# Performance work log

Measured on AMD Instinct MI355X. Metric: run time of the kernel, lower is better.

Reference implementation:

```python
import jax, jax.numpy as jnp
import numpy as np

N, D = 8192, 128

def setup_inputs() -> dict:
    key = jax.random.key(0)
    kq, kk, kv = jax.random.split(key, 3)
    query = jax.random.normal(kq, (N, D), dtype=jnp.float32)
    key_t = jax.random.normal(kk, (N, D), dtype=jnp.float32)
    value = jax.random.normal(kv, (N, D), dtype=jnp.float32)
    return {"query": query, "key": key_t, "value": value}

def reference(query, key, value):
    # FlashAttention-2 online softmax over blocks is mathematically exact
    # softmax attention: out = softmax(Q K^T / sqrt(d)) V, no mask.
    d = query.shape[-1]
    scale = 1.0 / jnp.sqrt(jnp.asarray(d, dtype=query.dtype))
    scores = jnp.einsum('qd,kd->qk', query, key) * scale  # [n, n]
    probs = jax.nn.softmax(scores, axis=-1)
    return jnp.einsum('qk,kd->qd', probs, value)  # [n, d]
```

## Files before the change

### kernel.cpp

```cpp
#include <hip/hip_runtime.h>
#include <hip/hip_bf16.h>

#define ATTN_N 8192
#define ATTN_D 128
#define TKEYS 128
#define NTILES (ATTN_N / TKEYS)
#define TILE_ELEMS (TKEYS * ATTN_D)
#define QROWS 64
#define KTPB 32

typedef __bf16 bf16_t;
typedef bf16_t bf16x2 __attribute__((ext_vector_type(2)));
typedef bf16_t bf16x8 __attribute__((ext_vector_type(8)));
typedef float f32x4 __attribute__((ext_vector_type(4)));

#if __has_builtin(__builtin_amdgcn_exp2f)
#define EXP2(x) __builtin_amdgcn_exp2f(x)
#else
#define EXP2(x) __expf((x) * 0.6931471805599453f)
#endif

__device__ __forceinline__ void dma16(const bf16_t* g, bf16_t* l) {
  __builtin_amdgcn_global_load_lds(
      (const __attribute__((address_space(1))) void*)g,
      (__attribute__((address_space(3))) void*)l, 16, 0, 0);
}

__global__ void prep_kernel(const float* __restrict__ q,
                            const float* __restrict__ k,
                            const float* __restrict__ v,
                            bf16_t* __restrict__ qb,
                            bf16_t* __restrict__ kswz,
                            bf16_t* __restrict__ vtswz) {
  __shared__ bf16_t tile[64][72];
  const int bk = blockIdx.x;
  const int bd = blockIdx.y;
  const int t = threadIdx.x;
  const float sc = 0.12751744f;

  const int row_l = t >> 2;
  const int key = bk * 64 + row_l;
  const int kt = key >> 7;
  const int r = key & 127;

#pragma unroll
  for (int u = 0; u < 2; ++u) {
    const int j = bd * 8 + (t & 3) * 2 + u;
    const float4* qs = (const float4*)(q + (size_t)key * ATTN_D + j * 8);
    const float4* ks = (const float4*)(k + (size_t)key * ATTN_D + j * 8);
    float4 a0 = qs[0], a1 = qs[1];
    float4 b0 = ks[0], b1 = ks[1];
    bf16x8 qo, ko;
    qo[0] = (bf16_t)(a0.x * sc); qo[1] = (bf16_t)(a0.y * sc);
    qo[2] = (bf16_t)(a0.z * sc); qo[3] = (bf16_t)(a0.w * sc);
    qo[4] = (bf16_t)(a1.x * sc); qo[5] = (bf16_t)(a1.y * sc);
    qo[6] = (bf16_t)(a1.z * sc); qo[7] = (bf16_t)(a1.w * sc);
    ko[0] = (bf16_t)b0.x; ko[1] = (bf16_t)b0.y;
    ko[2] = (bf16_t)b0.z; ko[3] = (bf16_t)b0.w;
    ko[4] = (bf16_t)b1.x; ko[5] = (bf16_t)b1.y;
    ko[6] = (bf16_t)b1.z; ko[7] = (bf16_t)b1.w;
    *(bf16x8*)(qb + (size_t)key * ATTN_D + j * 8) = qo;
    *(bf16x8*)(kswz + (size_t)kt * TILE_ELEMS + r * ATTN_D + (j ^ (r & 15)) * 8) = ko;
  }

  {
    const float* src = v + (size_t)key * ATTN_D + bd * 64 + (t & 3) * 16;
#pragma unroll
    for (int u = 0; u < 4; ++u) {
      float4 a = ((const float4*)src)[u];
      tile[row_l][(t & 3) * 16 + u * 4 + 0] = (bf16_t)a.x;
      tile[row_l][(t & 3) * 16 + u * 4 + 1] = (bf16_t)a.y;
      tile[row_l][(t & 3) * 16 + u * 4 + 2] = (bf16_t)a.z;
      tile[row_l][(t & 3) * 16 + u * 4 + 3] = (bf16_t)a.w;
    }
  }
  __syncthreads();
  {
    const int d_l = t >> 2;
    const int d = bd * 64 + d_l;
    const int h = bk & 1;
    const int ktv = bk >> 1;
#pragma unroll
    for (int u = 0; u < 2; ++u) {
      const int j = 8 * h + (t & 3) * 2 + u;
      bf16x8 o;
#pragma unroll
      for (int i = 0; i < 8; ++i) {
        const int key_tile = (j >> 2) * 32 + 4 * (j & 3) + (i >> 1) + 16 * (i & 1);
        o[i] = tile[key_tile - h * 64][d_l];
      }
      *(bf16x8*)(vtswz + (size_t)ktv * TILE_ELEMS + d * TKEYS + (j ^ (d & 15)) * 8) = o;
    }
  }
}

__global__ __launch_bounds__(512) void flash_attn_kernel(
    const bf16_t* __restrict__ qb, const bf16_t* __restrict__ kswz,
    const bf16_t* __restrict__ vtswz, float* __restrict__ partO,
    float* __restrict__ partL) {
  __shared__ __align__(16) bf16_t KV[2][2][TILE_ELEMS];
  __shared__ __align__(16) bf16_t Ps[8][32][40];
  __shared__ float cmb[8][32];
  float* Ob = (float*)&KV[0][0][0];

  const int t = threadIdx.x;
  const int w = t >> 6;
  const int lane = t & 63;
  const int quad = lane >> 4;
  const int col = lane & 15;
  const int rowHalf = w & 1;
  const int keyQ = w >> 1;
  const int blk = blockIdx.x;
  const int qg = blk >> 1;
  const int kh = blk & 1;
  const int q0 = qg * QROWS;
  const int ktbase = kh * KTPB;
  const int stg = ((blk >> 3) & 3) * 8;

  int offK[4][2], offV[8];
#pragma unroll
  for (int c = 0; c < 4; ++c)
#pragma unroll
    for (int cs = 0; cs < 2; ++cs)
      offK[c][cs] = (keyQ * 32 + cs * 16 + col) * ATTN_D +
                    (((c * 4 + quad) ^ col) * 8);
#pragma unroll
  for (int ds = 0; ds < 8; ++ds)
    offV[ds] = (ds * 16 + col) * TKEYS + (((keyQ * 4 + quad) ^ col) * 8);

  bf16x8 aq[2][4];
#pragma unroll
  for (int mi = 0; mi < 2; ++mi) {
    const int row = q0 + rowHalf * 32 + mi * 16 + col;
#pragma unroll
    for (int c = 0; c < 4; ++c)
      aq[mi][c] = *(const bf16x8*)(qb + (size_t)row * ATTN_D + c * 32 + quad * 8);
  }

  f32x4 oacc[2][8];
#pragma unroll
  for (int mi = 0; mi < 2; ++mi)
#pragma unroll
    for (int i = 0; i < 8; ++i) oacc[mi][i] = (f32x4){0.f, 0.f, 0.f, 0.f};
  float l_part[2][4] = {{0.f, 0.f, 0.f, 0.f}, {0.f, 0.f, 0.f, 0.f}};

  {
    const int kt = ktbase + (stg & (KTPB - 1));
    const bf16_t* kg = kswz + (size_t)kt * TILE_ELEMS + t * 8;
    const bf16_t* vg = vtswz + (size_t)kt * TILE_ELEMS + t * 8;
#pragma unroll
    for (int u = 0; u < 4; ++u) {
      dma16(kg + u * 4096, &KV[0][0][t * 8 + u * 4096]);
      dma16(vg + u * 4096, &KV[0][1][t * 8 + u * 4096]);
    }
  }
  __syncthreads();

  for (int it = 0; it < KTPB; ++it) {
    const int buf = it & 1;
    if (it + 1 < KTPB) {
      const int nt = ktbase + ((stg + it + 1) & (KTPB - 1));
      const bf16_t* kg = kswz + (size_t)nt * TILE_ELEMS + t * 8;
      const bf16_t* vg = vtswz + (size_t)nt * TILE_ELEMS + t * 8;
      bf16_t* kl = &KV[buf ^ 1][0][t * 8];
      bf16_t* vl = &KV[buf ^ 1][1][t * 8];
#pragma unroll
      for (int u = 0; u < 4; ++u) {
        dma16(kg + u * 4096, kl + u * 4096);
        dma16(vg + u * 4096, vl + u * 4096);
      }
    }
    const bf16_t* Kb = KV[buf][0];
    const bf16_t* Vb = KV[buf][1];

    f32x4 s[2][2];
#pragma unroll
    for (int mi = 0; mi < 2; ++mi)
#pragma unroll
      for (int ni = 0; ni < 2; ++ni) s[mi][ni] = (f32x4){0.f, 0.f, 0.f, 0.f};
#pragma unroll
    for (int c = 0; c < 4; ++c) {
      bf16x8 b0 = *(const bf16x8*)(Kb + offK[c][0]);
      bf16x8 b1 = *(const bf16x8*)(Kb + offK[c][1]);
      s[0][0] = __builtin_amdgcn_mfma_f32_16x16x32_bf16(aq[0][c], b0, s[0][0], 0, 0, 0);
      s[1][0] = __builtin_amdgcn_mfma_f32_16x16x32_bf16(aq[1][c], b0, s[1][0], 0, 0, 0);
      s[0][1] = __builtin_amdgcn_mfma_f32_16x16x32_bf16(aq[0][c], b1, s[0][1], 0, 0, 0);
      s[1][1] = __builtin_amdgcn_mfma_f32_16x16x32_bf16(aq[1][c], b1, s[1][1], 0, 0, 0);
    }

#pragma unroll
    for (int mi = 0; mi < 2; ++mi)
#pragma unroll
      for (int r = 0; r < 4; ++r) {
        float p0 = EXP2(s[mi][0][r]);
        float p1 = EXP2(s[mi][1][r]);
        l_part[mi][r] += p0 + p1;
        *(bf16x2*)&Ps[w][mi * 16 + quad * 4 + r][col * 2] =
            (bf16x2){(bf16_t)p0, (bf16_t)p1};
      }

    bf16x8 ap0 = *(const bf16x8*)&Ps[w][col][quad * 8];
    bf16x8 ap1 = *(const bf16x8*)&Ps[w][16 + col][quad * 8];
#pragma unroll
    for (int ds = 0; ds < 8; ++ds) {
      bf16x8 bv = *(const bf16x8*)(Vb + offV[ds]);
      oacc[0][ds] = __builtin_amdgcn_mfma_f32_16x16x32_bf16(ap0, bv, oacc[0][ds], 0, 0, 0);
      oacc[1][ds] = __builtin_amdgcn_mfma_f32_16x16x32_bf16(ap1, bv, oacc[1][ds], 0, 0, 0);
    }
    __syncthreads();
  }

#pragma unroll
  for (int mi = 0; mi < 2; ++mi)
#pragma unroll
    for (int r = 0; r < 4; ++r) {
      float v = l_part[mi][r];
#pragma unroll
      for (int off = 1; off < 16; off <<= 1)
        v += __shfl_xor(v, off, 64);
      if (col == 0) cmb[w][mi * 16 + quad * 4 + r] = v;
    }
  __syncthreads();
  if (t < QROWS) {
    const int rh = t >> 5, rl = t & 31;
    partL[(size_t)blk * QROWS + t] = cmb[rh][rl] + cmb[2 + rh][rl] +
                                     cmb[4 + rh][rl] + cmb[6 + rh][rl];
  }

#pragma unroll
  for (int p = 0; p < 4; ++p) {
    if (keyQ == p) {
#pragma unroll
      for (int mi = 0; mi < 2; ++mi)
#pragma unroll
        for (int ds = 0; ds < 8; ++ds)
#pragma unroll
          for (int r = 0; r < 4; ++r) {
            const int row = rowHalf * 32 + mi * 16 + quad * 4 + r;
            if (p == 0)
              Ob[row * 132 + ds * 16 + col] = oacc[mi][ds][r];
            else
              Ob[row * 132 + ds * 16 + col] += oacc[mi][ds][r];
          }
    }
    __syncthreads();
  }

  {
    float* dst = partO + (size_t)blk * (QROWS * ATTN_D);
    const int row = t >> 3;
    const int c0 = (t & 7) * 16;
#pragma unroll
    for (int u = 0; u < 4; ++u) {
      float4 vv = *(float4*)&Ob[row * 132 + c0 + u * 4];
      *(float4*)(dst + row * ATTN_D + c0 + u * 4) = vv;
    }
  }
}

__global__ void merge_kernel(const float* __restrict__ partO,
                             const float* __restrict__ partL,
                             float* __restrict__ out) {
  const int idx = blockIdx.x * blockDim.x + threadIdx.x;
  const int row = idx >> 5;
  const int gi = row >> 6;
  const int rl = row & 63;
  const int li = rl * 32 + (idx & 31);
  const float4* p0 = (const float4*)(partO + (size_t)(2 * gi) * (QROWS * ATTN_D));
  const float4* p1 = (const float4*)(partO + (size_t)(2 * gi + 1) * (QROWS * ATTN_D));
  const float invL = 1.0f / (partL[(size_t)(2 * gi) * QROWS + rl] +
                             partL[(size_t)(2 * gi + 1) * QROWS + rl]);
  float4 a = p0[li], b = p1[li], o;
  o.x = (a.x + b.x) * invL;
  o.y = (a.y + b.y) * invL;
  o.z = (a.z + b.z) * invL;
  o.w = (a.w + b.w) * invL;
  ((float4*)out)[idx] = o;
}

extern "C" void kernel_launch(void* const* d_in, const int* in_sizes, int n_in,
                              void* d_out, int out_size, void* d_ws, size_t ws_size,
                              hipStream_t stream) {
  const float* q = (const float*)d_in[0];
  const float* k = (const float*)d_in[1];
  const float* v = (const float*)d_in[2];
  float* out = (float*)d_out;

  bf16_t* qb = (bf16_t*)d_ws;
  bf16_t* kswz = qb + (size_t)ATTN_N * ATTN_D;
  bf16_t* vtswz = kswz + (size_t)ATTN_N * ATTN_D;
  float* partO = (float*)(vtswz + (size_t)ATTN_N * ATTN_D);
  float* partL = partO + (size_t)256 * QROWS * ATTN_D;

  prep_kernel<<<dim3(ATTN_N / 64, 2), 256, 0, stream>>>(q, k, v, qb, kswz, vtswz);
  flash_attn_kernel<<<256, 512, 0, stream>>>(qb, kswz, vtswz, partO, partL);
  merge_kernel<<<(ATTN_N * ATTN_D / 4) / 256, 256, 0, stream>>>(partO, partL, out);
}
```

Before: 123.9 us.

## Double query rows per block and split keys four ways

Each block now handles 128 query rows instead of 64, and the key range is split into 4 chunks instead of 2. This keeps the block count the same while each K/V tile in LDS is reused across twice as many query rows, which roughly halves K/V traffic per unit of work. The merge kernel now sums four partials. In exchange, per-thread accumulator registers double, which may reduce occupancy or cause spills, and the partial-output buffer and merge traffic grow.

```diff
diff --git a/kernel.cpp b/kernel.cpp
--- a/kernel.cpp
+++ b/kernel.cpp
@@ -6,8 +6,9 @@
 #define TKEYS 128
 #define NTILES (ATTN_N / TKEYS)
 #define TILE_ELEMS (TKEYS * ATTN_D)
-#define QROWS 64
-#define KTPB 32
+#define QROWS 128
+#define NSPLIT 4
+#define KTPB (NTILES / NSPLIT)
 
 typedef __bf16 bf16_t;
 typedef bf16_t bf16x2 __attribute__((ext_vector_type(2)));
@@ -100,7 +101,7 @@
     float* __restrict__ partL) {
   __shared__ __align__(16) bf16_t KV[2][2][TILE_ELEMS];
   __shared__ __align__(16) bf16_t Ps[8][32][40];
-  __shared__ float cmb[8][32];
+  __shared__ float cmb[8][64];
   float* Ob = (float*)&KV[0][0][0];
 
   const int t = threadIdx.x;
@@ -108,14 +109,14 @@
   const int lane = t & 63;
   const int quad = lane >> 4;
   const int col = lane & 15;
-  const int rowHalf = w & 1;
+  const int rowG = w & 1;
   const int keyQ = w >> 1;
   const int blk = blockIdx.x;
-  const int qg = blk >> 1;
-  const int kh = blk & 1;
+  const int qg = blk >> 2;
+  const int kh = blk & 3;
   const int q0 = qg * QROWS;
   const int ktbase = kh * KTPB;
-  const int stg = ((blk >> 3) & 3) * 8;
+  const int stg = ((blk >> 3) & 3) * 4;
 
   int offK[4][2], offV[8];
 #pragma unroll
@@ -128,21 +129,25 @@
   for (int ds = 0; ds < 8; ++ds)
     offV[ds] = (ds * 16 + col) * TKEYS + (((keyQ * 4 + quad) ^ col) * 8);
 
-  bf16x8 aq[2][4];
-#pragma unroll
-  for (int mi = 0; mi < 2; ++mi) {
-    const int row = q0 + rowHalf * 32 + mi * 16 + col;
+  bf16x8 aq[4][4];
+#pragma unroll
+  for (int mi = 0; mi < 4; ++mi) {
+    const int row = q0 + rowG * 64 + mi * 16 + col;
 #pragma unroll
     for (int c = 0; c < 4; ++c)
       aq[mi][c] = *(const bf16x8*)(qb + (size_t)row * ATTN_D + c * 32 + quad * 8);
   }
 
-  f32x4 oacc[2][8];
-#pragma unroll
-  for (int mi = 0; mi < 2; ++mi)
+  f32x4 oacc[4][8];
+#pragma unroll
+  for (int mi = 0; mi < 4; ++mi)
 #pragma unroll
     for (int i = 0; i < 8; ++i) oacc[mi][i] = (f32x4){0.f, 0.f, 0.f, 0.f};
-  float l_part[2][4] = {{0.f, 0.f, 0.f, 0.f}, {0.f, 0.f, 0.f, 0.f}};
+  float l_part[4][4];
+#pragma unroll
+  for (int mi = 0; mi < 4; ++mi)
+#pragma unroll
+    for (int r = 0; r < 4; ++r) l_part[mi][r] = 0.f;
 
   {
     const int kt = ktbase + (stg & (KTPB - 1));
@@ -173,45 +178,53 @@
     const bf16_t* Kb = KV[buf][0];
     const bf16_t* Vb = KV[buf][1];
 
-    f32x4 s[2][2];
-#pragma unroll
-    for (int mi = 0; mi < 2; ++mi)
+    f32x4 s[4][2];
+#pragma unroll
+    for (int mi = 0; mi < 4; ++mi)
 #pragma unroll
       for (int ni = 0; ni < 2; ++ni) s[mi][ni] = (f32x4){0.f, 0.f, 0.f, 0.f};
 #pragma unroll
     for (int c = 0; c < 4; ++c) {
       bf16x8 b0 = *(const bf16x8*)(Kb + offK[c][0]);
       bf16x8 b1 = *(const bf16x8*)(Kb + offK[c][1]);
-      s[0][0] = __builtin_amdgcn_mfma_f32_16x16x32_bf16(aq[0][c], b0, s[0][0], 0, 0, 0);
-      s[1][0] = __builtin_amdgcn_mfma_f32_16x16x32_bf16(aq[1][c], b0, s[1][0], 0, 0, 0);
-      s[0][1] = __builtin_amdgcn_mfma_f32_16x16x32_bf16(aq[0][c], b1, s[0][1], 0, 0, 0);
-      s[1][1] = __builtin_amdgcn_mfma_f32_16x16x32_bf16(aq[1][c], b1, s[1][1], 0, 0, 0);
-    }
-
-#pragma unroll
-    for (int mi = 0; mi < 2; ++mi)
-#pragma unroll
-      for (int r = 0; r < 4; ++r) {
-        float p0 = EXP2(s[mi][0][r]);
-        float p1 = EXP2(s[mi][1][r]);
-        l_part[mi][r] += p0 + p1;
-        *(bf16x2*)&Ps[w][mi * 16 + quad * 4 + r][col * 2] =
-            (bf16x2){(bf16_t)p0, (bf16_t)p1};
+#pragma unroll
+      for (int mi = 0; mi < 4; ++mi)
+        s[mi][0] = __builtin_amdgcn_mfma_f32_16x16x32_bf16(aq[mi][c], b0, s[mi][0], 0, 0, 0);
+#pragma unroll
+      for (int mi = 0; mi < 4; ++mi)
+        s[mi][1] = __builtin_amdgcn_mfma_f32_16x16x32_bf16(aq[mi][c], b1, s[mi][1], 0, 0, 0);
+    }
+
+#pragma unroll
+    for (int g = 0; g < 2; ++g) {
+#pragma unroll
+      for (int mj = 0; mj < 2; ++mj) {
+        const int mi = 2 * g + mj;
+#pragma unroll
+        for (int r = 0; r < 4; ++r) {
+          float p0 = EXP2(s[mi][0][r]);
+          float p1 = EXP2(s[mi][1][r]);
+          l_part[mi][r] += p0 + p1;
+          *(bf16x2*)&Ps[w][mj * 16 + quad * 4 + r][col * 2] =
+              (bf16x2){(bf16_t)p0, (bf16_t)p1};
+        }
       }
-
-    bf16x8 ap0 = *(const bf16x8*)&Ps[w][col][quad * 8];
-    bf16x8 ap1 = *(const bf16x8*)&Ps[w][16 + col][quad * 8];
-#pragma unroll
-    for (int ds = 0; ds < 8; ++ds) {
-      bf16x8 bv = *(const bf16x8*)(Vb + offV[ds]);
-      oacc[0][ds] = __builtin_amdgcn_mfma_f32_16x16x32_bf16(ap0, bv, oacc[0][ds], 0, 0, 0);
-      oacc[1][ds] = __builtin_amdgcn_mfma_f32_16x16x32_bf16(ap1, bv, oacc[1][ds], 0, 0, 0);
+      bf16x8 ap0 = *(const bf16x8*)&Ps[w][col][quad * 8];
+      bf16x8 ap1 = *(const bf16x8*)&Ps[w][16 + col][quad * 8];
+#pragma unroll
+      for (int ds = 0; ds < 8; ++ds) {
+        bf16x8 bv = *(const bf16x8*)(Vb + offV[ds]);
+        oacc[2 * g][ds] =
+            __builtin_amdgcn_mfma_f32_16x16x32_bf16(ap0, bv, oacc[2 * g][ds], 0, 0, 0);
+        oacc[2 * g + 1][ds] =
+            __builtin_amdgcn_mfma_f32_16x16x32_bf16(ap1, bv, oacc[2 * g + 1][ds], 0, 0, 0);
+      }
     }
     __syncthreads();
   }
 
 #pragma unroll
-  for (int mi = 0; mi < 2; ++mi)
+  for (int mi = 0; mi < 4; ++mi)
 #pragma unroll
     for (int r = 0; r < 4; ++r) {
       float v = l_part[mi][r];
@@ -222,21 +235,21 @@
     }
   __syncthreads();
   if (t < QROWS) {
-    const int rh = t >> 5, rl = t & 31;
-    partL[(size_t)blk * QROWS + t] = cmb[rh][rl] + cmb[2 + rh][rl] +
-                                     cmb[4 + rh][rl] + cmb[6 + rh][rl];
+    const int rg = t >> 6, rl = t & 63;
+    partL[(size_t)blk * QROWS + t] = cmb[rg][rl] + cmb[rg + 2][rl] +
+                                     cmb[rg + 4][rl] + cmb[rg + 6][rl];
   }
 
 #pragma unroll
   for (int p = 0; p < 4; ++p) {
     if (keyQ == p) {
 #pragma unroll
-      for (int mi = 0; mi < 2; ++mi)
+      for (int mi = 0; mi < 4; ++mi)
 #pragma unroll
         for (int ds = 0; ds < 8; ++ds)
 #pragma unroll
           for (int r = 0; r < 4; ++r) {
-            const int row = rowHalf * 32 + mi * 16 + quad * 4 + r;
+            const int row = rowG * 64 + mi * 16 + quad * 4 + r;
             if (p == 0)
               Ob[row * 132 + ds * 16 + col] = oacc[mi][ds][r];
             else
@@ -248,10 +261,10 @@
 
   {
     float* dst = partO + (size_t)blk * (QROWS * ATTN_D);
-    const int row = t >> 3;
-    const int c0 = (t & 7) * 16;
-#pragma unroll
-    for (int u = 0; u < 4; ++u) {
+    const int row = t >> 2;
+    const int c0 = (t & 3) * 32;
+#pragma unroll
+    for (int u = 0; u < 8; ++u) {
       float4 vv = *(float4*)&Ob[row * 132 + c0 + u * 4];
       *(float4*)(dst + row * ATTN_D + c0 + u * 4) = vv;
     }
@@ -263,18 +276,21 @@
                              float* __restrict__ out) {
   const int idx = blockIdx.x * blockDim.x + threadIdx.x;
   const int row = idx >> 5;
-  const int gi = row >> 6;
-  const int rl = row & 63;
+  const int gi = row >> 7;
+  const int rl = row & 127;
   const int li = rl * 32 + (idx & 31);
-  const float4* p0 = (const float4*)(partO + (size_t)(2 * gi) * (QROWS * ATTN_D));
-  const float4* p1 = (const float4*)(partO + (size_t)(2 * gi + 1) * (QROWS * ATTN_D));
-  const float invL = 1.0f / (partL[(size_t)(2 * gi) * QROWS + rl] +
-                             partL[(size_t)(2 * gi + 1) * QROWS + rl]);
-  float4 a = p0[li], b = p1[li], o;
-  o.x = (a.x + b.x) * invL;
-  o.y = (a.y + b.y) * invL;
-  o.z = (a.z + b.z) * invL;
-  o.w = (a.w + b.w) * invL;
+  float L = 0.f;
+  float4 o = {0.f, 0.f, 0.f, 0.f};
+#pragma unroll
+  for (int j = 0; j < NSPLIT; ++j) {
+    const int blk = gi * NSPLIT + j;
+    const float4 a =
+        ((const float4*)(partO + (size_t)blk * (QROWS * ATTN_D)))[li];
+    L += partL[(size_t)blk * QROWS + rl];
+    o.x += a.x; o.y += a.y; o.z += a.z; o.w += a.w;
+  }
+  const float invL = 1.0f / L;
+  o.x *= invL; o.y *= invL; o.z *= invL; o.w *= invL;
   ((float4*)out)[idx] = o;
 }
 
```

New measurement: 135.8 us. +9.6%, slower.
